# Performance work log

Measured on AMD Instinct MI355X. Metric: run time of the kernel, lower is better.

Reference implementation:

```python
import jax, jax.numpy as jnp
import numpy as np


def setup_inputs() -> dict:
    key = jax.random.key(0)
    k1, k2, k3, k4 = jax.random.split(key, 4)
    B, C, H, Wd = 32, 512, 32, 32
    sparse_dim, dict_size, feature_dim = 1024, 1024, 512
    x = jax.random.normal(k1, (B, C, H, Wd), dtype=jnp.float32)
    dictionary = jax.random.normal(k2, (dict_size, feature_dim), dtype=jnp.float32)
    # scale W, S like the LISTA init (|| . || ~ O(1)) so iterates stay bounded
    W = jax.random.normal(k3, (sparse_dim, feature_dim), dtype=jnp.float32) * 0.02
    S = jax.random.normal(k4, (sparse_dim, sparse_dim), dtype=jnp.float32) * 0.02
    thresh = jnp.float32(0.1)
    return {"x": x, "dictionary": dictionary, "W": W, "S": S, "thresh": thresh, "num_steps": 5}


def _soft_threshold(z, thresh):
    return jnp.sign(z) * jnp.maximum(jnp.abs(z) - thresh, 0.0)


def reference(x, dictionary, W, S, thresh, num_steps):
    B, C, H, Wd = x.shape
    sparse_dim = S.shape[0]
    # [B,C,H,W] -> [B*H*W, C]
    x_flat = jnp.transpose(x, (0, 2, 3, 1)).reshape(-1, C)
    dict_norm = dictionary / jnp.linalg.norm(dictionary, axis=1, keepdims=True)
    # W @ x^T is loop-invariant; compute once. [K, N]
    Wx = W @ x_flat.T
    z = jnp.zeros((sparse_dim, x_flat.shape[0]), dtype=x.dtype)
    for _ in range(num_steps):
        z = z + Wx
        z = z - S @ z
        z = _soft_threshold(z, thresh)
    # [K,N] -> [B,K,H,W]
    z = jnp.transpose(z.T.reshape(B, H, Wd, sparse_dim), (0, 3, 1, 2))
    return (z, dict_norm)
```

## Files before the change

kernel.cpp:

```cpp
#include <hip/hip_runtime.h>
#include <hip/hip_bf16.h>

typedef __bf16 bf16_t;
typedef __bf16 bf16x8 __attribute__((ext_vector_type(8)));
typedef float f32x4 __attribute__((ext_vector_type(4)));

#define GLOAD_LDS16(g, l)                                                      \
  __builtin_amdgcn_global_load_lds(                                            \
      (const __attribute__((address_space(1))) void*)(g),                      \
      (__attribute__((address_space(3))) void*)(l), 16, 0, 0)

#define MFMA(a, b, c) __builtin_amdgcn_mfma_f32_16x16x32_bf16((a), (b), (c), 0, 0, 0)

__global__ __launch_bounds__(512, 4) void gemm_kernel(
    const bf16_t* __restrict__ A, const bf16_t* __restrict__ Bt,
    int Kd, int mode,
    const bf16_t* __restrict__ WxIn, bf16_t* __restrict__ UnextOrWx,
    float* __restrict__ Out, const float* __restrict__ thresh_p)
{
  __shared__ __align__(16) char smem[49152];
  bf16_t* lds = (bf16_t*)smem;

  const int tid = threadIdx.x;
  const int wid = tid >> 6, lane = tid & 63;
  const int wr = wid >> 2, wc = wid & 3;
  const int lr = lane & 15, kg = lane >> 4;

  const int per = gridDim.x >> 3;
  const int logical = (blockIdx.x & 7) * per + (blockIdx.x >> 3);
  const int tileN = (logical & 3) << 8;
  const int tileM = (logical >> 2) << 7;
  const int NT = Kd >> 5;

  const int l4 = tid & 3, t2 = tid >> 2;
  const int rowA = t2;
  const int kcsA = l4 ^ ((rowA >> 1) & 3);
  const size_t offA = (size_t)(tileM + rowA) * Kd + kcsA * 8;

  auto stageA = [&](int t, int buf) {
    GLOAD_LDS16(A + offA + (t << 5), lds + buf * 12288 + tid * 8);
  };
  auto stageB = [&](int t, int g, int buf) {
    const int col = (t2 >> 5) * 64 + g * 32 + (t2 & 31);
    const int kcs = l4 ^ ((col >> 1) & 3);
    GLOAD_LDS16(Bt + (size_t)(tileN + col) * Kd + (t << 5) + kcs * 8,
                lds + buf * 12288 + 4096 + col * 32 + l4 * 8);
  };
  auto readA = [&](int mi, int buf) -> bf16x8 {
    const int R = wr * 64 + mi * 16 + lr;
    return *(const bf16x8*)(lds + buf * 12288 + R * 32 + ((kg ^ ((R >> 1) & 3)) << 3));
  };
  auto readB = [&](int ni, int buf) -> bf16x8 {
    const int C = wc * 64 + ni * 16 + lr;
    return *(const bf16x8*)(lds + buf * 12288 + 4096 + C * 32 + ((kg ^ ((C >> 1) & 3)) << 3));
  };

  f32x4 acc[4][4] = {};
  bf16x8 af[2], b0[2], b1[2];

  stageA(0, 0); stageB(0, 0, 0); stageB(0, 1, 0);
  asm volatile("s_waitcnt vmcnt(1)" ::: "memory");
  __builtin_amdgcn_s_barrier();

  for (int t = 0; t < NT; ++t) {
    const int cur = t & 1, nxt = cur ^ 1;
    const int tn = (t + 1 == NT) ? 0 : t + 1;

    af[0] = readA(0, cur); af[1] = readA(1, cur);
    b0[0] = readB(0, cur); b0[1] = readB(1, cur);
    stageA(tn, nxt);
    asm volatile("s_waitcnt lgkmcnt(0)" ::: "memory");
    __builtin_amdgcn_sched_barrier(0);
    __builtin_amdgcn_s_setprio(1);
    acc[0][0] = MFMA(af[0], b0[0], acc[0][0]);
    acc[0][1] = MFMA(af[0], b0[1], acc[0][1]);
    acc[1][0] = MFMA(af[1], b0[0], acc[1][0]);
    acc[1][1] = MFMA(af[1], b0[1], acc[1][1]);
    __builtin_amdgcn_s_setprio(0);
    asm volatile("s_waitcnt vmcnt(1)" ::: "memory");
    __builtin_amdgcn_s_barrier();

    b1[0] = readB(2, cur); b1[1] = readB(3, cur);
    stageB(tn, 0, nxt);
    asm volatile("s_waitcnt lgkmcnt(0)" ::: "memory");
    __builtin_amdgcn_sched_barrier(0);
    __builtin_amdgcn_s_setprio(1);
    acc[0][2] = MFMA(af[0], b1[0], acc[0][2]);
    acc[0][3] = MFMA(af[0], b1[1], acc[0][3]);
    acc[1][2] = MFMA(af[1], b1[0], acc[1][2]);
    acc[1][3] = MFMA(af[1], b1[1], acc[1][3]);
    __builtin_amdgcn_s_setprio(0);

    af[0] = readA(2, cur); af[1] = readA(3, cur);
    stageB(tn, 1, nxt);
    asm volatile("s_waitcnt lgkmcnt(0)" ::: "memory");
    __builtin_amdgcn_sched_barrier(0);
    __builtin_amdgcn_s_setprio(1);
    acc[2][2] = MFMA(af[0], b1[0], acc[2][2]);
    acc[2][3] = MFMA(af[0], b1[1], acc[2][3]);
    acc[3][2] = MFMA(af[1], b1[0], acc[3][2]);
    acc[3][3] = MFMA(af[1], b1[1], acc[3][3]);
    __builtin_amdgcn_s_setprio(0);

    __builtin_amdgcn_s_setprio(1);
    acc[2][0] = MFMA(af[0], b0[0], acc[2][0]);
    acc[2][1] = MFMA(af[0], b0[1], acc[2][1]);
    acc[3][0] = MFMA(af[1], b0[0], acc[3][0]);
    acc[3][1] = MFMA(af[1], b0[1], acc[3][1]);
    __builtin_amdgcn_s_setprio(0);
    asm volatile("s_waitcnt vmcnt(1)" ::: "memory");
    __builtin_amdgcn_s_barrier();
  }

  const float th = *thresh_p;

  if (mode <= 1) {
    asm volatile("s_waitcnt vmcnt(0)" ::: "memory");
    __syncthreads();
    float* Tl = (float*)smem;
    #pragma unroll
    for (int half = 0; half < 2; ++half) {
      #pragma unroll
      for (int mc = 0; mc < 2; ++mc) {
        if (half | mc) __syncthreads();
        if (wr == half) {
          #pragma unroll
          for (int mj = 0; mj < 2; ++mj) {
            const int mi = mc * 2 + mj;
            const int rl = mj * 16 + kg * 4;
            #pragma unroll
            for (int ni = 0; ni < 4; ++ni) {
              const int cl = wc * 64 + ni * 16 + lr;
              #pragma unroll
              for (int r = 0; r < 4; ++r)
                Tl[(rl + r) * 260 + cl] = acc[mi][ni][r];
            }
          }
        }
        __syncthreads();
        #pragma unroll
        for (int j = 0; j < 2; ++j) {
          const int chunk = j * 512 + tid;
          const int rl = chunk >> 5;
          const int c8 = (chunk & 31) * 8;
          float v[8];
          *(f32x4*)&v[0] = *(const f32x4*)&Tl[rl * 260 + c8];
          *(f32x4*)&v[4] = *(const f32x4*)&Tl[rl * 260 + c8 + 4];
          const int grow = tileM + half * 64 + mc * 32 + rl;
          const size_t gidx = (size_t)grow * 1024 + tileN + c8;
          bf16x8 ov;
          if (mode == 1) {
            const bf16x8 wx = *(const bf16x8*)&WxIn[gidx];
            #pragma unroll
            for (int e = 0; e < 8; ++e) {
              const float a  = fabsf(v[e]) - th;
              const float zn = (a > 0.f) ? copysignf(a, v[e]) : 0.f;
              ov[e] = (bf16_t)(zn + (float)wx[e]);
            }
          } else {
            #pragma unroll
            for (int e = 0; e < 8; ++e) ov[e] = (bf16_t)v[e];
          }
          *(bf16x8*)&UnextOrWx[gidx] = ov;
        }
      }
    }
  } else {
    #pragma unroll
    for (int mi = 0; mi < 4; ++mi)
      #pragma unroll
      for (int ni = 0; ni < 4; ++ni)
        #pragma unroll
        for (int r = 0; r < 4; ++r) {
          const float v = acc[mi][ni][r];
          const float a = fabsf(v) - th;
          acc[mi][ni][r] = (a > 0.f) ? copysignf(a, v) : 0.f;
        }
    asm volatile("s_waitcnt vmcnt(0)" ::: "memory");
    __syncthreads();
    float* T = (float*)smem;
    const int    bb    = tileM >> 10;
    const size_t obase = (size_t)bb * 1048576 + (size_t)(tileM & 1023);
    for (int ch = 0; ch < 8; ++ch) {
      if (ch) __syncthreads();
      if (wc == (ch >> 1)) {
        #pragma unroll
        for (int nj = 0; nj < 2; ++nj) {
          const int ni = (ch & 1) * 2 + nj;
          const int cp = nj * 16 + lr;
          #pragma unroll
          for (int mi = 0; mi < 4; ++mi)
            #pragma unroll
            for (int r = 0; r < 4; ++r)
              T[cp * 132 + wr * 64 + mi * 16 + kg * 4 + r] = acc[mi][ni][r];
        }
      }
      __syncthreads();
      #pragma unroll
      for (int j = 0; j < 2; ++j) {
        const int f  = tid + j * 512;
        const int cp = f >> 5;
        const int R4 = (f & 31) * 4;
        const f32x4 v = *(const f32x4*)&T[cp * 132 + R4];
        *(f32x4*)&Out[obase + (size_t)(tileN + ch * 32 + cp) * 1024 + R4] = v;
      }
    }
  }
}

__global__ void cast_f32_bf16_kernel(const float* __restrict__ src,
                                     bf16_t* __restrict__ dst, int n) {
  int i = blockIdx.x * blockDim.x + threadIdx.x;
  if (i < n) dst[i] = (bf16_t)src[i];
}

__global__ void make_T_kernel(const float* __restrict__ S,
                              bf16_t* __restrict__ T) {
  const int idx = blockIdx.x * blockDim.x + threadIdx.x;
  const int i = idx >> 10, j = idx & 1023;
  T[idx] = (bf16_t)(((i == j) ? 1.0f : 0.0f) - S[idx]);
}

__global__ void transpose_cast_x_kernel(const float* __restrict__ x,
                                        bf16_t* __restrict__ xt) {
  __shared__ float t[32][33];
  const int b  = blockIdx.z;
  const int p0 = blockIdx.x * 32;
  const int c0 = blockIdx.y * 32;
  const int tx = threadIdx.x, ty = threadIdx.y;
  #pragma unroll
  for (int i = 0; i < 32; i += 8)
    t[ty + i][tx] = x[((size_t)b * 512 + c0 + ty + i) * 1024 + p0 + tx];
  __syncthreads();
  #pragma unroll
  for (int i = 0; i < 32; i += 8)
    xt[((size_t)b * 1024 + p0 + ty + i) * 512 + c0 + tx] = (bf16_t)t[tx][ty + i];
}

__global__ void dict_norm_kernel(const float* __restrict__ dict,
                                 float* __restrict__ out) {
  const int row = blockIdx.x;
  const int tid = threadIdx.x;
  const float* r = dict + (size_t)row * 512;
  float s = 0.f;
  for (int i = tid; i < 512; i += 256) { float v = r[i]; s += v * v; }
  #pragma unroll
  for (int off = 32; off > 0; off >>= 1) s += __shfl_down(s, off);
  __shared__ float ps[4];
  if ((tid & 63) == 0) ps[tid >> 6] = s;
  __syncthreads();
  const float inv = 1.0f / sqrtf(ps[0] + ps[1] + ps[2] + ps[3]);
  for (int i = tid; i < 512; i += 256) out[(size_t)row * 512 + i] = r[i] * inv;
}

extern "C" void kernel_launch(void* const* d_in, const int* in_sizes, int n_in,
                              void* d_out, int out_size, void* d_ws, size_t ws_size,
                              hipStream_t stream) {
  const float* x      = (const float*)d_in[0];
  const float* dict   = (const float*)d_in[1];
  const float* W      = (const float*)d_in[2];
  const float* S      = (const float*)d_in[3];
  const float* thresh = (const float*)d_in[4];

  float* out = (float*)d_out;

  char* ws = (char*)d_ws;
  bf16_t* uA   = (bf16_t*)ws;
  bf16_t* uB   = (bf16_t*)(ws + 67108864);
  bf16_t* WxBf = (bf16_t*)(ws + 134217728);
  bf16_t* xt   = (bf16_t*)(ws + 201326592);
  bf16_t* Wbf  = (bf16_t*)(ws + 234881024);
  bf16_t* Tbf  = (bf16_t*)(ws + 235929600);

  float* dnorm = out + 33554432;

  cast_f32_bf16_kernel<<<dim3(2048), dim3(256), 0, stream>>>(W, Wbf, 524288);
  make_T_kernel<<<dim3(2048), dim3(512), 0, stream>>>(S, Tbf);
  transpose_cast_x_kernel<<<dim3(32, 16, 32), dim3(32, 8), 0, stream>>>(x, xt);
  dict_norm_kernel<<<dim3(1024), dim3(256), 0, stream>>>(dict, dnorm);

  gemm_kernel<<<dim3(1024), dim3(512), 0, stream>>>(
      xt, Wbf, 512, 0, nullptr, WxBf, nullptr, thresh);

  bf16_t* uc = WxBf; bf16_t* un = uA;
  for (int s = 0; s < 4; ++s) {
    gemm_kernel<<<dim3(1024), dim3(512), 0, stream>>>(
        uc, Tbf, 1024, 1, WxBf, un, nullptr, thresh);
    uc = un;
    un = (uc == uA) ? uB : uA;
  }
  gemm_kernel<<<dim3(1024), dim3(512), 0, stream>>>(
      uc, Tbf, 1024, 2, nullptr, nullptr, out, thresh);
}
```

Before: 591.9 us.

## Switch GEMM to 256x128 tiles with BK=64 and triple-buffered LDS pipeline

The GEMM tile becomes 256 rows by 128 columns with an 8x... (4x2) wave grid. The K step per iteration doubles to 64, and LDS grows to three stages so loads are issued two tiles ahead. The swizzle and the epilogues are rewritten to match the new tile shape. The aim is to cut barrier overhead per MFMA and hide global latency better, at the cost of fewer resident blocks per CU (launch bounds drop from 4 to 2) because of the much larger LDS footprint.

```diff
diff --git a/kernel.cpp b/kernel.cpp
--- a/kernel.cpp
+++ b/kernel.cpp
@@ -2,6 +2,7 @@
 #include <hip/hip_bf16.h>
 
 typedef __bf16 bf16_t;
+typedef __bf16 bf16x4 __attribute__((ext_vector_type(4)));
 typedef __bf16 bf16x8 __attribute__((ext_vector_type(8)));
 typedef float f32x4 __attribute__((ext_vector_type(4)));
 
@@ -12,104 +13,119 @@
 
 #define MFMA(a, b, c) __builtin_amdgcn_mfma_f32_16x16x32_bf16((a), (b), (c), 0, 0, 0)
 
-__global__ __launch_bounds__(512, 4) void gemm_kernel(
+__global__ __launch_bounds__(512, 2) void gemm_kernel(
     const bf16_t* __restrict__ A, const bf16_t* __restrict__ Bt,
     int Kd, int mode,
     const bf16_t* __restrict__ WxIn, bf16_t* __restrict__ UnextOrWx,
     float* __restrict__ Out, const float* __restrict__ thresh_p)
 {
-  __shared__ __align__(16) char smem[49152];
+  __shared__ __align__(16) char smem[147456];
   bf16_t* lds = (bf16_t*)smem;
 
   const int tid = threadIdx.x;
   const int wid = tid >> 6, lane = tid & 63;
-  const int wr = wid >> 2, wc = wid & 3;
+  const int wr = wid >> 1, wc = wid & 1;
   const int lr = lane & 15, kg = lane >> 4;
 
   const int per = gridDim.x >> 3;
   const int logical = (blockIdx.x & 7) * per + (blockIdx.x >> 3);
-  const int tileN = (logical & 3) << 8;
-  const int tileM = (logical >> 2) << 7;
-  const int NT = Kd >> 5;
-
-  const int l4 = tid & 3, t2 = tid >> 2;
-  const int rowA = t2;
-  const int kcsA = l4 ^ ((rowA >> 1) & 3);
-  const size_t offA = (size_t)(tileM + rowA) * Kd + kcsA * 8;
-
-  auto stageA = [&](int t, int buf) {
-    GLOAD_LDS16(A + offA + (t << 5), lds + buf * 12288 + tid * 8);
+  const int tileN = (logical & 7) << 7;
+  const int tileM = (logical >> 3) << 8;
+  const int NT = Kd >> 6;
+
+  size_t offA[4]; int dstA[4];
+  #pragma unroll
+  for (int j = 0; j < 4; ++j) {
+    const int f = j * 512 + tid;
+    const int row = f >> 3, u = f & 7;
+    const int ug = u ^ (row & 7);
+    offA[j] = (size_t)(tileM + row) * Kd + ug * 8;
+    dstA[j] = f * 8;
+  }
+  size_t offB[2]; int dstB[2];
+  #pragma unroll
+  for (int j = 0; j < 2; ++j) {
+    const int f = j * 512 + tid;
+    const int col = f >> 3, u = f & 7;
+    const int ug = u ^ (col & 7);
+    offB[j] = (size_t)(tileN + col) * Kd + ug * 8;
+    dstB[j] = 16384 + f * 8;
+  }
+
+  auto readA = [&](int mi, int ks, int bs) -> bf16x8 {
+    const int R = wr * 64 + mi * 16 + lr;
+    const int ul = (ks * 4 + kg) ^ (R & 7);
+    return *(const bf16x8*)(lds + bs + R * 64 + ul * 8);
   };
-  auto stageB = [&](int t, int g, int buf) {
-    const int col = (t2 >> 5) * 64 + g * 32 + (t2 & 31);
-    const int kcs = l4 ^ ((col >> 1) & 3);
-    GLOAD_LDS16(Bt + (size_t)(tileN + col) * Kd + (t << 5) + kcs * 8,
-                lds + buf * 12288 + 4096 + col * 32 + l4 * 8);
+  auto readB = [&](int ni, int ks, int bs) -> bf16x8 {
+    const int C = wc * 64 + ni * 16 + lr;
+    const int ul = (ks * 4 + kg) ^ (C & 7);
+    return *(const bf16x8*)(lds + bs + 16384 + C * 64 + ul * 8);
   };
-  auto readA = [&](int mi, int buf) -> bf16x8 {
-    const int R = wr * 64 + mi * 16 + lr;
-    return *(const bf16x8*)(lds + buf * 12288 + R * 32 + ((kg ^ ((R >> 1) & 3)) << 3));
-  };
-  auto readB = [&](int ni, int buf) -> bf16x8 {
-    const int C = wc * 64 + ni * 16 + lr;
-    return *(const bf16x8*)(lds + buf * 12288 + 4096 + C * 32 + ((kg ^ ((C >> 1) & 3)) << 3));
-  };
 
   f32x4 acc[4][4] = {};
-  bf16x8 af[2], b0[2], b1[2];
-
-  stageA(0, 0); stageB(0, 0, 0); stageB(0, 1, 0);
-  asm volatile("s_waitcnt vmcnt(1)" ::: "memory");
+  bf16x8 af[4], bfr[4];
+
+  #pragma unroll
+  for (int j = 0; j < 4; ++j) GLOAD_LDS16(A + offA[j], lds + dstA[j]);
+  #pragma unroll
+  for (int j = 0; j < 2; ++j) GLOAD_LDS16(Bt + offB[j], lds + dstB[j]);
+  if (NT > 1) {
+    #pragma unroll
+    for (int j = 0; j < 4; ++j) GLOAD_LDS16(A + offA[j] + 64, lds + 24576 + dstA[j]);
+    #pragma unroll
+    for (int j = 0; j < 2; ++j) GLOAD_LDS16(Bt + offB[j] + 64, lds + 24576 + dstB[j]);
+  }
+  asm volatile("s_waitcnt vmcnt(6)" ::: "memory");
   __builtin_amdgcn_s_barrier();
 
+  int buf = 0, sb3 = 2;
   for (int t = 0; t < NT; ++t) {
-    const int cur = t & 1, nxt = cur ^ 1;
-    const int tn = (t + 1 == NT) ? 0 : t + 1;
-
-    af[0] = readA(0, cur); af[1] = readA(1, cur);
-    b0[0] = readB(0, cur); b0[1] = readB(1, cur);
-    stageA(tn, nxt);
+    const int bs = buf * 24576;
+    const int sbs = sb3 * 24576;
+    const int ts = (t + 2 < NT) ? t + 2 : t + 2 - NT;
+    const size_t ko = (size_t)ts << 6;
+
+    #pragma unroll
+    for (int mi = 0; mi < 4; ++mi) af[mi] = readA(mi, 0, bs);
+    #pragma unroll
+    for (int ni = 0; ni < 4; ++ni) bfr[ni] = readB(ni, 0, bs);
+    GLOAD_LDS16(A + offA[0] + ko, lds + sbs + dstA[0]);
+    GLOAD_LDS16(A + offA[1] + ko, lds + sbs + dstA[1]);
+    GLOAD_LDS16(A + offA[2] + ko, lds + sbs + dstA[2]);
+    __builtin_amdgcn_s_barrier();
     asm volatile("s_waitcnt lgkmcnt(0)" ::: "memory");
     __builtin_amdgcn_sched_barrier(0);
     __builtin_amdgcn_s_setprio(1);
-    acc[0][0] = MFMA(af[0], b0[0], acc[0][0]);
-    acc[0][1] = MFMA(af[0], b0[1], acc[0][1]);
-    acc[1][0] = MFMA(af[1], b0[0], acc[1][0]);
-    acc[1][1] = MFMA(af[1], b0[1], acc[1][1]);
+    #pragma unroll
+    for (int mi = 0; mi < 4; ++mi)
+      #pragma unroll
+      for (int ni = 0; ni < 4; ++ni)
+        acc[mi][ni] = MFMA(af[mi], bfr[ni], acc[mi][ni]);
     __builtin_amdgcn_s_setprio(0);
-    asm volatile("s_waitcnt vmcnt(1)" ::: "memory");
+
+    #pragma unroll
+    for (int mi = 0; mi < 4; ++mi) af[mi] = readA(mi, 1, bs);
+    #pragma unroll
+    for (int ni = 0; ni < 4; ++ni) bfr[ni] = readB(ni, 1, bs);
+    GLOAD_LDS16(A + offA[3] + ko, lds + sbs + dstA[3]);
+    GLOAD_LDS16(Bt + offB[0] + ko, lds + sbs + dstB[0]);
+    GLOAD_LDS16(Bt + offB[1] + ko, lds + sbs + dstB[1]);
     __builtin_amdgcn_s_barrier();
-
-    b1[0] = readB(2, cur); b1[1] = readB(3, cur);
-    stageB(tn, 0, nxt);
     asm volatile("s_waitcnt lgkmcnt(0)" ::: "memory");
     __builtin_amdgcn_sched_barrier(0);
     __builtin_amdgcn_s_setprio(1);
-    acc[0][2] = MFMA(af[0], b1[0], acc[0][2]);
-    acc[0][3] = MFMA(af[0], b1[1], acc[0][3]);
-    acc[1][2] = MFMA(af[1], b1[0], acc[1][2]);
-    acc[1][3] = MFMA(af[1], b1[1], acc[1][3]);
+    #pragma unroll
+    for (int mi = 0; mi < 4; ++mi)
+      #pragma unroll
+      for (int ni = 0; ni < 4; ++ni)
+        acc[mi][ni] = MFMA(af[mi], bfr[ni], acc[mi][ni]);
     __builtin_amdgcn_s_setprio(0);
-
-    af[0] = readA(2, cur); af[1] = readA(3, cur);
-    stageB(tn, 1, nxt);
-    asm volatile("s_waitcnt lgkmcnt(0)" ::: "memory");
-    __builtin_amdgcn_sched_barrier(0);
-    __builtin_amdgcn_s_setprio(1);
-    acc[2][2] = MFMA(af[0], b1[0], acc[2][2]);
-    acc[2][3] = MFMA(af[0], b1[1], acc[2][3]);
-    acc[3][2] = MFMA(af[1], b1[0], acc[3][2]);
-    acc[3][3] = MFMA(af[1], b1[1], acc[3][3]);
-    __builtin_amdgcn_s_setprio(0);
-
-    __builtin_amdgcn_s_setprio(1);
-    acc[2][0] = MFMA(af[0], b0[0], acc[2][0]);
-    acc[2][1] = MFMA(af[0], b0[1], acc[2][1]);
-    acc[3][0] = MFMA(af[1], b0[0], acc[3][0]);
-    acc[3][1] = MFMA(af[1], b0[1], acc[3][1]);
-    __builtin_amdgcn_s_setprio(0);
-    asm volatile("s_waitcnt vmcnt(1)" ::: "memory");
+    asm volatile("s_waitcnt vmcnt(6)" ::: "memory");
     __builtin_amdgcn_s_barrier();
+
+    buf = (buf == 2) ? 0 : buf + 1;
+    sb3 = (sb3 == 2) ? 0 : sb3 + 1;
   }
 
   const float th = *thresh_p;
@@ -119,50 +135,45 @@
     __syncthreads();
     float* Tl = (float*)smem;
     #pragma unroll
-    for (int half = 0; half < 2; ++half) {
-      #pragma unroll
-      for (int mc = 0; mc < 2; ++mc) {
-        if (half | mc) __syncthreads();
-        if (wr == half) {
+    for (int c = 0; c < 8; ++c) {
+      if (c) __syncthreads();
+      if (wr == (c >> 1)) {
+        #pragma unroll
+        for (int mj = 0; mj < 2; ++mj) {
+          const int mi = (c & 1) * 2 + mj;
+          const int rl = mj * 16 + kg * 4;
           #pragma unroll
-          for (int mj = 0; mj < 2; ++mj) {
-            const int mi = mc * 2 + mj;
-            const int rl = mj * 16 + kg * 4;
+          for (int ni = 0; ni < 4; ++ni) {
+            const int cl = wc * 64 + ni * 16 + lr;
             #pragma unroll
-            for (int ni = 0; ni < 4; ++ni) {
-              const int cl = wc * 64 + ni * 16 + lr;
-              #pragma unroll
-              for (int r = 0; r < 4; ++r)
-                Tl[(rl + r) * 260 + cl] = acc[mi][ni][r];
-            }
+            for (int r = 0; r < 4; ++r)
+              Tl[(rl + r) * 132 + cl] = acc[mi][ni][r];
           }
         }
-        __syncthreads();
-        #pragma unroll
-        for (int j = 0; j < 2; ++j) {
-          const int chunk = j * 512 + tid;
-          const int rl = chunk >> 5;
-          const int c8 = (chunk & 31) * 8;
-          float v[8];
-          *(f32x4*)&v[0] = *(const f32x4*)&Tl[rl * 260 + c8];
-          *(f32x4*)&v[4] = *(const f32x4*)&Tl[rl * 260 + c8 + 4];
-          const int grow = tileM + half * 64 + mc * 32 + rl;
-          const size_t gidx = (size_t)grow * 1024 + tileN + c8;
-          bf16x8 ov;
-          if (mode == 1) {
-            const bf16x8 wx = *(const bf16x8*)&WxIn[gidx];
-            #pragma unroll
-            for (int e = 0; e < 8; ++e) {
-              const float a  = fabsf(v[e]) - th;
-              const float zn = (a > 0.f) ? copysignf(a, v[e]) : 0.f;
-              ov[e] = (bf16_t)(zn + (float)wx[e]);
-            }
-          } else {
-            #pragma unroll
-            for (int e = 0; e < 8; ++e) ov[e] = (bf16_t)v[e];
+      }
+      __syncthreads();
+      #pragma unroll
+      for (int j = 0; j < 2; ++j) {
+        const int f  = j * 512 + tid;
+        const int rl = f >> 5;
+        const int c4 = (f & 31) * 4;
+        const f32x4 v = *(const f32x4*)&Tl[rl * 132 + c4];
+        const int grow = tileM + c * 32 + rl;
+        const size_t gidx = (size_t)grow * 1024 + tileN + c4;
+        bf16x4 ov;
+        if (mode == 1) {
+          const bf16x4 wx = *(const bf16x4*)&WxIn[gidx];
+          #pragma unroll
+          for (int e = 0; e < 4; ++e) {
+            const float a  = fabsf(v[e]) - th;
+            const float zn = (a > 0.f) ? copysignf(a, v[e]) : 0.f;
+            ov[e] = (bf16_t)(zn + (float)wx[e]);
           }
-          *(bf16x8*)&UnextOrWx[gidx] = ov;
+        } else {
+          #pragma unroll
+          for (int e = 0; e < 4; ++e) ov[e] = (bf16_t)v[e];
         }
+        *(bf16x4*)&UnextOrWx[gidx] = ov;
       }
     }
   } else {
@@ -181,7 +192,8 @@
     float* T = (float*)smem;
     const int    bb    = tileM >> 10;
     const size_t obase = (size_t)bb * 1048576 + (size_t)(tileM & 1023);
-    for (int ch = 0; ch < 8; ++ch) {
+    #pragma unroll
+    for (int ch = 0; ch < 4; ++ch) {
       if (ch) __syncthreads();
       if (wc == (ch >> 1)) {
         #pragma unroll
@@ -192,17 +204,17 @@
           for (int mi = 0; mi < 4; ++mi)
             #pragma unroll
             for (int r = 0; r < 4; ++r)
-              T[cp * 132 + wr * 64 + mi * 16 + kg * 4 + r] = acc[mi][ni][r];
+              T[cp * 260 + wr * 64 + mi * 16 + kg * 4 + r] = acc[mi][ni][r];
         }
       }
       __syncthreads();
       #pragma unroll
-      for (int j = 0; j < 2; ++j) {
-        const int f  = tid + j * 512;
-        const int cp = f >> 5;
-        const int R4 = (f & 31) * 4;
-        const f32x4 v = *(const f32x4*)&T[cp * 132 + R4];
-        *(f32x4*)&Out[obase + (size_t)(tileN + ch * 32 + cp) * 1024 + R4] = v;
+      for (int j = 0; j < 4; ++j) {
+        const int f  = j * 512 + tid;
+        const int cp = f >> 6;
+        const int p4 = (f & 63) * 4;
+        const f32x4 v = *(const f32x4*)&T[cp * 260 + p4];
+        *(f32x4*)&Out[obase + (size_t)(tileN + ch * 32 + cp) * 1024 + p4] = v;
       }
     }
   }
```

Result: faster. 550.1 us (-7.1%).
